# Optimization experiments

Hardware: AMD Instinct MI355X
Metric: run time of the kernel (lower is better)

The kernel has to match this reference:

```python
import jax, jax.numpy as jnp
import numpy as np

B, L, H, E = 8, 1024, 8, 64
HIST = 512


def setup_inputs() -> dict:
    key = jax.random.key(0)
    ks = jax.random.split(key, 6)
    shp = (B, L, H, E)
    q, k, v, qd, kd, vd = (jax.random.normal(kk, shp, dtype=jnp.float32) for kk in ks)
    # DoubleTriangularCausalMask surrogate: strictly-upper-triangular causal mask (diagonal=1)
    attn_mask = jnp.triu(jnp.ones((L, L), dtype=bool), k=1)[None, None]  # (1,1,L,S)
    return {
        "queries": q, "keys": k, "values": v,
        "queries_drawn": qd, "keys_drawn": kd, "values_drawn": vd,
        "attn_mask": attn_mask, "history_len": HIST,
    }


def reference(queries, keys, values, queries_drawn, keys_drawn, values_drawn, attn_mask, history_len):
    # drawn_y=True branch of FullFixedTimeCausalConstructiveAttention with history_len set.
    B, L, H, E = queries.shape
    scale = 1.0 / float(np.sqrt(E))
    hist = history_len
    idx = jnp.arange(hist, L)

    # queries[:, hist:] = queries_drawn[:, hist:]
    q_eff = jnp.concatenate([queries[:, :hist], queries_drawn[:, hist:]], axis=1)

    scores = jnp.einsum('blhe,bshe->bhls', q_eff, keys)  # (B,H,L,S)
    # diagonal positions l>=hist use drawn keys: q_eff[l] . keys_drawn[l]
    diag_scores = jnp.einsum('blhe,blhe->bhl', q_eff[:, hist:], keys_drawn[:, hist:])
    scores = scores.at[:, :, idx, idx].set(diag_scores)

    scores = jnp.where(attn_mask, -jnp.inf, scores)
    A = jax.nn.softmax(scale * scores, axis=-1)  # (B,H,L,S); dropout rate 0 in eval

    # values substitution on the diagonal (l==s, l>=hist) is a rank-1 correction;
    # avoids materializing the torch (B,H,D,L,S) repeated tensor.
    V = jnp.einsum('bhls,bshd->blhd', A, values)
    diag_A = A[:, :, idx, idx]                      # (B,H,L-hist)
    delta = values_drawn[:, hist:] - values[:, hist:]  # (B,L-hist,H,D)
    V = V.at[:, hist:].add(jnp.transpose(diag_A, (0, 2, 1))[..., None] * delta)
    return V
```

## Files before the change

### kernel.cpp

```cpp
#include <hip/hip_runtime.h>

#define BB   8
#define LL   1024
#define HH   8
#define EE   64
#define HIST 512
#define KSTR 72

#define SCALE2 0.18033688011112043f

typedef _Float16 f16;
typedef _Float16 v8h   __attribute__((ext_vector_type(8)));
typedef _Float16 f16x2 __attribute__((ext_vector_type(2)));
typedef _Float16 f16x4 __attribute__((ext_vector_type(4)));
typedef float    v4f   __attribute__((ext_vector_type(4)));

__device__ __forceinline__ float fexp2(float x) {
#if __has_builtin(__builtin_amdgcn_exp2f)
  return __builtin_amdgcn_exp2f(x);
#else
  return __expf(x * 0.6931471805599453f);
#endif
}

__device__ __forceinline__ void load16f(const float* __restrict__ p, float* __restrict__ f) {
  const float4* p4 = reinterpret_cast<const float4*>(p);
  float4 a = p4[0], b = p4[1], c = p4[2], d = p4[3];
  f[0]=a.x;  f[1]=a.y;  f[2]=a.z;  f[3]=a.w;
  f[4]=b.x;  f[5]=b.y;  f[6]=b.z;  f[7]=b.w;
  f[8]=c.x;  f[9]=c.y;  f[10]=c.z; f[11]=c.w;
  f[12]=d.x; f[13]=d.y; f[14]=d.z; f[15]=d.w;
}

__device__ __forceinline__ void load8f(const float* __restrict__ p, float* __restrict__ f) {
  const float4* p4 = reinterpret_cast<const float4*>(p);
  float4 a = p4[0], b = p4[1];
  f[0]=a.x; f[1]=a.y; f[2]=a.z; f[3]=a.w;
  f[4]=b.x; f[5]=b.y; f[6]=b.z; f[7]=b.w;
}

struct TileState {
  v4f   o[4];
  float m, l, pd;
};

__device__ __forceinline__ void tile_update(
    TileState& st, const v8h* __restrict__ qf, bool dt, bool drawn,
    const f16* __restrict__ Ks, const f16* __restrict__ Vt,
    f16* __restrict__ Psw, const float* __restrict__ zd,
    int w, int ln, int lq)
{
  v4f S[4];
#pragma unroll
  for (int nb = 0; nb < 4; ++nb) {
    const f16* krow = &Ks[(nb * 16 + ln) * KSTR + 8 * lq];
    v8h k0 = *reinterpret_cast<const v8h*>(krow);
    v8h k1 = *reinterpret_cast<const v8h*>(krow + 32);
    v4f acc = (v4f){0.f, 0.f, 0.f, 0.f};
    acc = __builtin_amdgcn_mfma_f32_16x16x32_f16(k0, qf[0], acc, 0, 0, 0);
    acc = __builtin_amdgcn_mfma_f32_16x16x32_f16(k1, qf[1], acc, 0, 0, 0);
    S[nb] = acc;
  }

  float z[4][4];
#pragma unroll
  for (int nb = 0; nb < 4; ++nb)
#pragma unroll
    for (int r = 0; r < 4; ++r) z[nb][r] = S[nb][r] * SCALE2;

  const int qlocal = w * 16 + ln;
  if (dt) {
#pragma unroll
    for (int nb = 0; nb < 4; ++nb) {
#pragma unroll
      for (int r = 0; r < 4; ++r) {
        const int klocal = nb * 16 + lq * 4 + r;
        if (klocal > qlocal)                 z[nb][r] = -1e30f;
        else if (drawn && klocal == qlocal)  z[nb][r] = zd[qlocal];
      }
    }
  }

  float a0 = fmaxf(fmaxf(z[0][0], z[0][1]), fmaxf(z[0][2], z[0][3]));
  float a1 = fmaxf(fmaxf(z[1][0], z[1][1]), fmaxf(z[1][2], z[1][3]));
  float a2 = fmaxf(fmaxf(z[2][0], z[2][1]), fmaxf(z[2][2], z[2][3]));
  float a3 = fmaxf(fmaxf(z[3][0], z[3][1]), fmaxf(z[3][2], z[3][3]));
  float mx = fmaxf(fmaxf(a0, a1), fmaxf(a2, a3));
  mx = fmaxf(mx, __shfl_xor(mx, 16));
  mx = fmaxf(mx, __shfl_xor(mx, 32));

  const float mn = fmaxf(st.m, mx);
  const float al = fexp2(st.m - mn);
  st.m = mn;

  float p[4][4], rsum = 0.f, pdl = 0.f;
#pragma unroll
  for (int nb = 0; nb < 4; ++nb) {
#pragma unroll
    for (int r = 0; r < 4; ++r) {
      const float pv = fexp2(z[nb][r] - mn);
      p[nb][r] = pv;
      rsum += pv;
      if (dt && drawn && (nb * 16 + lq * 4 + r) == qlocal) pdl = pv;
    }
  }
  rsum += __shfl_xor(rsum, 16);
  rsum += __shfl_xor(rsum, 32);
  if (dt && drawn) {
    pdl += __shfl_xor(pdl, 16);
    pdl += __shfl_xor(pdl, 32);
    st.pd = pdl;
  }
  st.l = st.l * al + rsum;

  float alO[4];
#pragma unroll
  for (int r = 0; r < 4; ++r) alO[r] = __shfl(al, lq * 4 + r);
#pragma unroll
  for (int nb = 0; nb < 4; ++nb)
#pragma unroll
    for (int r = 0; r < 4; ++r) st.o[nb][r] *= alO[r];

#pragma unroll
  for (int nb = 0; nb < 4; ++nb) {
    f16x4 pk;
#pragma unroll
    for (int r = 0; r < 4; ++r) pk[r] = (f16)p[nb][r];
    *reinterpret_cast<f16x4*>(&Psw[ln * KSTR + nb * 16 + lq * 4]) = pk;
  }
  v8h pA0 = *reinterpret_cast<const v8h*>(&Psw[ln * KSTR + 8 * lq]);
  v8h pA1 = *reinterpret_cast<const v8h*>(&Psw[ln * KSTR + 32 + 8 * lq]);

#pragma unroll
  for (int nb = 0; nb < 4; ++nb) {
    const int d   = nb * 16 + ln;
    const int dsw = (d >> 3) & 7;
    const f16* vbase = &Vt[d * KSTR];
    v8h v0 = *reinterpret_cast<const v8h*>(vbase + (((lq    ) ^ dsw) & 7) * 8);
    v8h v1 = *reinterpret_cast<const v8h*>(vbase + (((lq + 4) ^ dsw) & 7) * 8);
    st.o[nb] = __builtin_amdgcn_mfma_f32_16x16x32_f16(pA0, v0, st.o[nb], 0, 0, 0);
    st.o[nb] = __builtin_amdgcn_mfma_f32_16x16x32_f16(pA1, v1, st.o[nb], 0, 0, 0);
  }
}

extern "C" __global__ __launch_bounds__(256, 4)
void ftcca_split(const float* __restrict__ Q,  const float* __restrict__ K,
                 const float* __restrict__ V,  const float* __restrict__ Qd,
                 const float* __restrict__ Kd, const float* __restrict__ Vd,
                 float* __restrict__ out)
{
  __shared__ f16   Ks[64 * KSTR];
  __shared__ f16   Vt[64 * KSTR];
  __shared__ f16   Ps[4][16 * KSTR];
  __shared__ float zdiag[64];

  const int bh  = blockIdx.x & 63;
  const int a   = blockIdx.x >> 6;
  const int qt  = 15 - a;
  const bool drawn = (qt >= 8);
  const int b   = bh >> 3, h = bh & 7;
  const int t   = threadIdx.x;
  const int w    = t >> 6;
  const int lane = t & 63;
  const int ln   = lane & 15;
  const int lq   = lane >> 4;
  const int rs   = t >> 2;
  const int es0  = (t & 3) * 16;
  const int vr0  = (t >> 3) * 2;
  const int vd0  = (t & 7) * 8;

  const size_t base = ((size_t)b * LL * HH + h) * EE;
  const int ROWF = HH * EE;

  if (drawn) {
    const int l = qt * 64 + rs;
    const float* qrow = Qd + base + (size_t)l * ROWF + es0;
    const float* krow = Kd + base + (size_t)l * ROWF + es0;
    float par = 0.f;
#pragma unroll
    for (int i = 0; i < 16; ++i) par += qrow[i] * krow[i];
    par += __shfl_xor(par, 1);
    par += __shfl_xor(par, 2);
    if ((t & 3) == 0) zdiag[rs] = SCALE2 * par;
  }

  const int rowt_q = w * 16 + ln;
  const float* qsrc = drawn ? Qd : Q;
  v8h qf[2];
  {
    const float* pq = qsrc + base + (size_t)(qt * 64 + rowt_q) * ROWF;
#pragma unroll
    for (int c = 0; c < 2; ++c) {
      const float* x = pq + 32 * c + 8 * lq;
#pragma unroll
      for (int j = 0; j < 8; ++j) qf[c][j] = (f16)x[j];
    }
  }

  TileState st;
#pragma unroll
  for (int nb = 0; nb < 4; ++nb) st.o[nb] = (v4f){0, 0, 0, 0};
  st.m = -1e30f; st.l = 0.f; st.pd = 0.f;

  float tk[16], tv[16];
  load16f(K + base + (size_t)rs * ROWF + es0, tk);
  load8f(V + base + (size_t)vr0 * ROWF + vd0, tv);
  load8f(V + base + (size_t)(vr0 + 1) * ROWF + vd0, tv + 8);

  for (int i = 0; i <= qt; ++i) {
    __syncthreads();
    {
      v8h k0, k1;
#pragma unroll
      for (int j = 0; j < 8; ++j) { k0[j] = (f16)tk[j]; k1[j] = (f16)tk[8 + j]; }
      v8h* kd0 = reinterpret_cast<v8h*>(&Ks[rs * KSTR + es0]);
      kd0[0] = k0;
      kd0[1] = k1;
      const int vswz = vr0 >> 3;
#pragma unroll
      for (int dd = 0; dd < 8; ++dd) {
        const int d  = vd0 + dd;
        const int ch = (vswz ^ (d >> 3)) & 7;
        f16x2 val; val[0] = (f16)tv[dd]; val[1] = (f16)tv[8 + dd];
        *reinterpret_cast<f16x2*>(&Vt[d * KSTR + ch * 8 + (vr0 & 7)]) = val;
      }
    }
    __syncthreads();

    if (i < qt) {
      const size_t r0 = (size_t)((i + 1) * 64);
      load16f(K + base + (r0 + rs) * ROWF + es0, tk);
      load8f(V + base + (r0 + vr0) * ROWF + vd0, tv);
      load8f(V + base + (r0 + vr0 + 1) * ROWF + vd0, tv + 8);
    }

    tile_update(st, qf, i == qt, drawn, Ks, Vt, Ps[w], zdiag, w, ln, lq);
  }

  float lO[4], inv[4], pdO[4];
#pragma unroll
  for (int r = 0; r < 4; ++r) lO[r] = __shfl(st.l, lq * 4 + r);
#pragma unroll
  for (int r = 0; r < 4; ++r) inv[r] = 1.f / lO[r];
  if (drawn) {
#pragma unroll
    for (int r = 0; r < 4; ++r) pdO[r] = __shfl(st.pd, lq * 4 + r);
  }

#pragma unroll
  for (int nb = 0; nb < 4; ++nb) {
    const int col = nb * 16 + ln;
#pragma unroll
    for (int r = 0; r < 4; ++r) {
      const int l = qt * 64 + w * 16 + lq * 4 + r;
      const size_t g = base + (size_t)l * ROWF + col;
      float val = st.o[nb][r] * inv[r];
      if (drawn) val += (pdO[r] * inv[r]) * (Vd[g] - V[g]);
      out[g] = val;
    }
  }
}

extern "C" void kernel_launch(void* const* d_in, const int* in_sizes, int n_in,
                              void* d_out, int out_size, void* d_ws, size_t ws_size,
                              hipStream_t stream) {
  const float* q  = (const float*)d_in[0];
  const float* k  = (const float*)d_in[1];
  const float* v  = (const float*)d_in[2];
  const float* qd = (const float*)d_in[3];
  const float* kd = (const float*)d_in[4];
  const float* vd = (const float*)d_in[5];
  float* out = (float*)d_out;

  ftcca_split<<<dim3(1024), dim3(256), 0, stream>>>(q, k, v, qd, kd, vd, out);
}
```

Baseline: 156.7 us.

## Keep softmax probabilities in registers via permuted key rows and transposed PV MFMA

Permutes the key rows fed to the QK^T MFMA so the probability accumulator layout already matches the operand layout the PV MFMA needs. The P tile no longer round-trips through shared memory, and the PV MFMA now has its operands swapped so the output is transposed per lane. Row statistics become per-lane, which removes the alpha and normaliser broadcasts and allows float4 output stores. Reductions use permlane swaps and packed f16 conversion with round-toward-zero, which changes rounding slightly.

```diff
diff --git a/kernel.cpp b/kernel.cpp
--- a/kernel.cpp
+++ b/kernel.cpp
@@ -1,25 +1,59 @@
 #include <hip/hip_runtime.h>
 
-#define BB   8
 #define LL   1024
 #define HH   8
 #define EE   64
-#define HIST 512
 #define KSTR 72
 
 #define SCALE2 0.18033688011112043f
 
 typedef _Float16 f16;
-typedef _Float16 v8h   __attribute__((ext_vector_type(8)));
-typedef _Float16 f16x2 __attribute__((ext_vector_type(2)));
-typedef _Float16 f16x4 __attribute__((ext_vector_type(4)));
-typedef float    v4f   __attribute__((ext_vector_type(4)));
+typedef _Float16 v8h  __attribute__((ext_vector_type(8)));
+typedef _Float16 h2   __attribute__((ext_vector_type(2)));
+typedef float    v4f  __attribute__((ext_vector_type(4)));
+typedef int      v2i  __attribute__((ext_vector_type(2)));
 
 __device__ __forceinline__ float fexp2(float x) {
 #if __has_builtin(__builtin_amdgcn_exp2f)
   return __builtin_amdgcn_exp2f(x);
 #else
   return __expf(x * 0.6931471805599453f);
+#endif
+}
+
+__device__ __forceinline__ h2 pkh2(float a, float b) {
+#if __has_builtin(__builtin_amdgcn_cvt_pkrtz)
+  return __builtin_bit_cast(h2, __builtin_amdgcn_cvt_pkrtz(a, b));
+#else
+  h2 r; r[0] = (f16)a; r[1] = (f16)b; return r;
+#endif
+}
+
+__device__ __forceinline__ float red4max(float x) {
+#if __has_builtin(__builtin_amdgcn_permlane16_swap) && __has_builtin(__builtin_amdgcn_permlane32_swap)
+  int xi = __float_as_int(x);
+  v2i a = __builtin_amdgcn_permlane16_swap(xi, xi, false, false);
+  float m = fmaxf(__int_as_float(a.x), __int_as_float(a.y));
+  int mi = __float_as_int(m);
+  v2i b = __builtin_amdgcn_permlane32_swap(mi, mi, false, false);
+  return fmaxf(__int_as_float(b.x), __int_as_float(b.y));
+#else
+  x = fmaxf(x, __shfl_xor(x, 16));
+  return fmaxf(x, __shfl_xor(x, 32));
+#endif
+}
+
+__device__ __forceinline__ float red4sum(float x) {
+#if __has_builtin(__builtin_amdgcn_permlane16_swap) && __has_builtin(__builtin_amdgcn_permlane32_swap)
+  int xi = __float_as_int(x);
+  v2i a = __builtin_amdgcn_permlane16_swap(xi, xi, false, false);
+  float s = __int_as_float(a.x) + __int_as_float(a.y);
+  int si = __float_as_int(s);
+  v2i b = __builtin_amdgcn_permlane32_swap(si, si, false, false);
+  return __int_as_float(b.x) + __int_as_float(b.y);
+#else
+  x += __shfl_xor(x, 16);
+  return x + __shfl_xor(x, 32);
 #endif
 }
 
@@ -47,13 +81,14 @@
 __device__ __forceinline__ void tile_update(
     TileState& st, const v8h* __restrict__ qf, bool dt, bool drawn,
     const f16* __restrict__ Ks, const f16* __restrict__ Vt,
-    f16* __restrict__ Psw, const float* __restrict__ zd,
-    int w, int ln, int lq)
+    const float* __restrict__ zd,
+    int w, int ln, int lq,
+    const int* __restrict__ rk, const int* __restrict__ kb)
 {
   v4f S[4];
 #pragma unroll
   for (int nb = 0; nb < 4; ++nb) {
-    const f16* krow = &Ks[(nb * 16 + ln) * KSTR + 8 * lq];
+    const f16* krow = &Ks[rk[nb] * KSTR + 8 * lq];
     v8h k0 = *reinterpret_cast<const v8h*>(krow);
     v8h k1 = *reinterpret_cast<const v8h*>(krow + 32);
     v4f acc = (v4f){0.f, 0.f, 0.f, 0.f};
@@ -70,13 +105,14 @@
 
   const int qlocal = w * 16 + ln;
   if (dt) {
+    const float zdq = drawn ? zd[qlocal] : 0.f;
 #pragma unroll
     for (int nb = 0; nb < 4; ++nb) {
 #pragma unroll
       for (int r = 0; r < 4; ++r) {
-        const int klocal = nb * 16 + lq * 4 + r;
-        if (klocal > qlocal)                 z[nb][r] = -1e30f;
-        else if (drawn && klocal == qlocal)  z[nb][r] = zd[qlocal];
+        const int kl = kb[nb] + r;
+        if (kl > qlocal)                 z[nb][r] = -1e30f;
+        else if (drawn && kl == qlocal)  z[nb][r] = zdq;
       }
     }
   }
@@ -85,9 +121,7 @@
   float a1 = fmaxf(fmaxf(z[1][0], z[1][1]), fmaxf(z[1][2], z[1][3]));
   float a2 = fmaxf(fmaxf(z[2][0], z[2][1]), fmaxf(z[2][2], z[2][3]));
   float a3 = fmaxf(fmaxf(z[3][0], z[3][1]), fmaxf(z[3][2], z[3][3]));
-  float mx = fmaxf(fmaxf(a0, a1), fmaxf(a2, a3));
-  mx = fmaxf(mx, __shfl_xor(mx, 16));
-  mx = fmaxf(mx, __shfl_xor(mx, 32));
+  const float mx = red4max(fmaxf(fmaxf(a0, a1), fmaxf(a2, a3)));
 
   const float mn = fmaxf(st.m, mx);
   const float al = fexp2(st.m - mn);
@@ -101,35 +135,33 @@
       const float pv = fexp2(z[nb][r] - mn);
       p[nb][r] = pv;
       rsum += pv;
-      if (dt && drawn && (nb * 16 + lq * 4 + r) == qlocal) pdl = pv;
-    }
-  }
-  rsum += __shfl_xor(rsum, 16);
-  rsum += __shfl_xor(rsum, 32);
-  if (dt && drawn) {
-    pdl += __shfl_xor(pdl, 16);
-    pdl += __shfl_xor(pdl, 32);
-    st.pd = pdl;
-  }
+      if (dt && drawn && (kb[nb] + r) == qlocal) pdl = pv;
+    }
+  }
+  rsum = red4sum(rsum);
+  if (dt && drawn) st.pd = red4sum(pdl);
   st.l = st.l * al + rsum;
-
-  float alO[4];
-#pragma unroll
-  for (int r = 0; r < 4; ++r) alO[r] = __shfl(al, lq * 4 + r);
 #pragma unroll
   for (int nb = 0; nb < 4; ++nb)
 #pragma unroll
-    for (int r = 0; r < 4; ++r) st.o[nb][r] *= alO[r];
-
-#pragma unroll
-  for (int nb = 0; nb < 4; ++nb) {
-    f16x4 pk;
-#pragma unroll
-    for (int r = 0; r < 4; ++r) pk[r] = (f16)p[nb][r];
-    *reinterpret_cast<f16x4*>(&Psw[ln * KSTR + nb * 16 + lq * 4]) = pk;
-  }
-  v8h pA0 = *reinterpret_cast<const v8h*>(&Psw[ln * KSTR + 8 * lq]);
-  v8h pA1 = *reinterpret_cast<const v8h*>(&Psw[ln * KSTR + 32 + 8 * lq]);
+    for (int r = 0; r < 4; ++r) st.o[nb][r] *= al;
+
+  h2 wq[4][2];
+#pragma unroll
+  for (int nb = 0; nb < 4; ++nb) {
+    wq[nb][0] = pkh2(p[nb][0], p[nb][1]);
+    wq[nb][1] = pkh2(p[nb][2], p[nb][3]);
+  }
+  const bool swp = (lq & 1);
+  union U8 { v8h v; h2 h[4]; } A0, A1;
+  A0.h[0] = swp ? wq[1][0] : wq[0][0];
+  A0.h[1] = swp ? wq[1][1] : wq[0][1];
+  A0.h[2] = swp ? wq[0][0] : wq[1][0];
+  A0.h[3] = swp ? wq[0][1] : wq[1][1];
+  A1.h[0] = swp ? wq[3][0] : wq[2][0];
+  A1.h[1] = swp ? wq[3][1] : wq[2][1];
+  A1.h[2] = swp ? wq[2][0] : wq[3][0];
+  A1.h[3] = swp ? wq[2][1] : wq[3][1];
 
 #pragma unroll
   for (int nb = 0; nb < 4; ++nb) {
@@ -138,8 +170,8 @@
     const f16* vbase = &Vt[d * KSTR];
     v8h v0 = *reinterpret_cast<const v8h*>(vbase + (((lq    ) ^ dsw) & 7) * 8);
     v8h v1 = *reinterpret_cast<const v8h*>(vbase + (((lq + 4) ^ dsw) & 7) * 8);
-    st.o[nb] = __builtin_amdgcn_mfma_f32_16x16x32_f16(pA0, v0, st.o[nb], 0, 0, 0);
-    st.o[nb] = __builtin_amdgcn_mfma_f32_16x16x32_f16(pA1, v1, st.o[nb], 0, 0, 0);
+    st.o[nb] = __builtin_amdgcn_mfma_f32_16x16x32_f16(v0, A0.v, st.o[nb], 0, 0, 0);
+    st.o[nb] = __builtin_amdgcn_mfma_f32_16x16x32_f16(v1, A1.v, st.o[nb], 0, 0, 0);
   }
 }
 
@@ -151,7 +183,6 @@
 {
   __shared__ f16   Ks[64 * KSTR];
   __shared__ f16   Vt[64 * KSTR];
-  __shared__ f16   Ps[4][16 * KSTR];
   __shared__ float zdiag[64];
 
   const int bh  = blockIdx.x & 63;
@@ -172,6 +203,17 @@
   const size_t base = ((size_t)b * LL * HH + h) * EE;
   const int ROWF = HH * EE;
 
+  const int q2 = ln >> 2;
+  int rk[4], kb[4];
+  rk[0] = ln + ((q2 + 1) >> 1) * 8;
+  rk[1] = ln + 4 + (q2 >> 1) * 8;
+  rk[2] = rk[0] + 32;
+  rk[3] = rk[1] + 32;
+  kb[0] = 4 * lq + ((lq + 1) >> 1) * 8;
+  kb[1] = 4 * lq + 4 + (lq >> 1) * 8;
+  kb[2] = kb[0] + 32;
+  kb[3] = kb[1] + 32;
+
   if (drawn) {
     const int l = qt * 64 + rs;
     const float* qrow = Qd + base + (size_t)l * ROWF + es0;
@@ -221,8 +263,8 @@
       for (int dd = 0; dd < 8; ++dd) {
         const int d  = vd0 + dd;
         const int ch = (vswz ^ (d >> 3)) & 7;
-        f16x2 val; val[0] = (f16)tv[dd]; val[1] = (f16)tv[8 + dd];
-        *reinterpret_cast<f16x2*>(&Vt[d * KSTR + ch * 8 + (vr0 & 7)]) = val;
+        h2 val; val[0] = (f16)tv[dd]; val[1] = (f16)tv[8 + dd];
+        *reinterpret_cast<h2*>(&Vt[d * KSTR + ch * 8 + (vr0 & 7)]) = val;
       }
     }
     __syncthreads();
@@ -234,30 +276,31 @@
       load8f(V + base + (r0 + vr0 + 1) * ROWF + vd0, tv + 8);
     }
 
-    tile_update(st, qf, i == qt, drawn, Ks, Vt, Ps[w], zdiag, w, ln, lq);
-  }
-
-  float lO[4], inv[4], pdO[4];
-#pragma unroll
-  for (int r = 0; r < 4; ++r) lO[r] = __shfl(st.l, lq * 4 + r);
-#pragma unroll
-  for (int r = 0; r < 4; ++r) inv[r] = 1.f / lO[r];
-  if (drawn) {
-#pragma unroll
-    for (int r = 0; r < 4; ++r) pdO[r] = __shfl(st.pd, lq * 4 + r);
-  }
-
-#pragma unroll
-  for (int nb = 0; nb < 4; ++nb) {
-    const int col = nb * 16 + ln;
-#pragma unroll
-    for (int r = 0; r < 4; ++r) {
-      const int l = qt * 64 + w * 16 + lq * 4 + r;
-      const size_t g = base + (size_t)l * ROWF + col;
-      float val = st.o[nb][r] * inv[r];
-      if (drawn) val += (pdO[r] * inv[r]) * (Vd[g] - V[g]);
-      out[g] = val;
-    }
+    tile_update(st, qf, i == qt, drawn, Ks, Vt, zdiag, w, ln, lq, rk, kb);
+  }
+
+  const float inv = 1.f / st.l;
+  const float pdinv = st.pd * inv;
+  const int lrow = qt * 64 + w * 16 + ln;
+
+#pragma unroll
+  for (int nb = 0; nb < 4; ++nb) {
+    const int d0 = nb * 16 + lq * 4;
+    const size_t g = base + (size_t)lrow * ROWF + d0;
+    float4 o4;
+    o4.x = st.o[nb][0] * inv;
+    o4.y = st.o[nb][1] * inv;
+    o4.z = st.o[nb][2] * inv;
+    o4.w = st.o[nb][3] * inv;
+    if (drawn) {
+      float4 vd4 = *reinterpret_cast<const float4*>(Vd + g);
+      float4 v4  = *reinterpret_cast<const float4*>(V + g);
+      o4.x += pdinv * (vd4.x - v4.x);
+      o4.y += pdinv * (vd4.y - v4.y);
+      o4.z += pdinv * (vd4.z - v4.z);
+      o4.w += pdinv * (vd4.w - v4.w);
+    }
+    *reinterpret_cast<float4*>(out + g) = o4;
   }
 }
 
```

Measured after the change: 155.5 us. Within noise of the previous version (-0.8%).
